# Optimization experiments

Measured on AMD Instinct MI355X. Metric: run time of the kernel, lower is better.

The kernel has to match this reference:

```python
import jax, jax.numpy as jnp
import numpy as np

DIM = 512
NUM_HEADS = 8
HEAD_DIM = DIM // NUM_HEADS
MAX_SIZE = 128


def setup_inputs() -> dict:
    key = jax.random.key(0)
    ks = jax.random.split(key, 13)
    B, C, H, W = 4, DIM, 128, 128
    inp = {
        "x": jax.random.normal(ks[0], (B, C, H, W), jnp.float32),
        "q_w": jax.random.normal(ks[1], (DIM, DIM), jnp.float32) * 0.02,
        "q_b": jax.random.normal(ks[2], (DIM,), jnp.float32) * 0.02,
        "k_w": jax.random.normal(ks[3], (DIM, DIM), jnp.float32) * 0.02,
        "k_b": jax.random.normal(ks[4], (DIM,), jnp.float32) * 0.02,
        "v_w": jax.random.normal(ks[5], (DIM, DIM), jnp.float32) * 0.02,
        "v_b": jax.random.normal(ks[6], (DIM,), jnp.float32) * 0.02,
        "o_w": jax.random.normal(ks[7], (DIM, DIM), jnp.float32) * 0.02,
        "o_b": jax.random.normal(ks[8], (DIM,), jnp.float32) * 0.02,
        "pos_q": jax.random.normal(ks[9], (1, NUM_HEADS, MAX_SIZE, HEAD_DIM), jnp.float32),
        "pos_k": jax.random.normal(ks[10], (1, NUM_HEADS, MAX_SIZE, HEAD_DIM), jnp.float32),
        "pos_v": jax.random.normal(ks[11], (1, NUM_HEADS, MAX_SIZE, HEAD_DIM), jnp.float32),
        "g_q": jnp.ones((1,), jnp.float32),
        "g_k": jnp.ones((1,), jnp.float32),
        "g_v1": jnp.ones((1,), jnp.float32),
        "g_v2": jnp.ones((1,), jnp.float32),
    }
    return inp


def _gated_axial_attn(x, q_w, q_b, k_w, k_b, v_w, v_b, o_w, o_b,
                      pos_q, pos_k, pos_v, g_q, g_k, g_v1, g_v2):
    B, C, H, W = x.shape
    nh, hd = NUM_HEADS, C // NUM_HEADS
    scale = hd ** (-0.5)
    # axis='width': attend along W for each (B,H) row
    xf = jnp.transpose(x, (0, 2, 3, 1)).reshape(B * H, W, C)  # (BH, W, C)

    def proj(w, b):
        y = xf @ w.T + b                       # (BH, W, C)
        return jnp.transpose(y.reshape(B * H, W, nh, hd), (0, 2, 1, 3))  # (BH, nh, W, hd)

    q = proj(q_w, q_b)
    k = proj(k_w, k_b)
    v = proj(v_w, v_b)

    pq = pos_q[0, :, :W, :]  # (nh, W, hd)
    pk = pos_k[0, :, :W, :]
    pv = pos_v[0, :, :W, :]

    # scores[i,j] = q_i.k_j + g_q * q_i.pq_j + g_k * pk_i.k_j, all scaled
    scores = jnp.einsum('bnid,bnjd->bnij', q, k)
    scores = scores + g_q[0] * jnp.einsum('bnid,njd->bnij', q, pq)
    scores = scores + g_k[0] * jnp.einsum('nid,bnjd->bnij', pk, k)
    attn = jax.nn.softmax(scores * scale, axis=-1)  # (BH, nh, W, W)

    vmix = g_v1[0] * v + g_v2[0] * pv[None]        # (BH, nh, W, hd)
    out = jnp.einsum('bnij,bnjd->bnid', attn, vmix)
    out = jnp.transpose(out, (0, 2, 1, 3)).reshape(B * H, W, C)
    out = out @ o_w.T + o_b
    return jnp.transpose(out.reshape(B, H, W, C), (0, 3, 1, 2))  # (B, C, H, W)


def reference(x, q_w, q_b, k_w, k_b, v_w, v_b, o_w, o_b,
              pos_q, pos_k, pos_v, g_q, g_k, g_v1, g_v2):
    return _gated_axial_attn(x, q_w, q_b, k_w, k_b, v_w, v_b, o_w, o_b,
                             pos_q, pos_k, pos_v, g_q, g_k, g_v1, g_v2)
```

## Files before the change

kernel.cpp:

```cpp
#include <hip/hip_runtime.h>

typedef __bf16 bf16;
typedef __attribute__((ext_vector_type(8))) __bf16 bf16x8;
typedef __attribute__((ext_vector_type(4))) __bf16 bf16x4;
typedef __attribute__((ext_vector_type(4))) float fvec4;

#define MFMA16(a, b, c) __builtin_amdgcn_mfma_f32_16x16x32_bf16(a, b, c, 0, 0, 0)

__device__ __forceinline__ void glds16(const bf16* g, bf16* l) {
  __builtin_amdgcn_global_load_lds(
      (const __attribute__((address_space(1))) void*)g,
      (__attribute__((address_space(3))) void*)l, 16, 0, 0);
}

__device__ inline fvec4 zero4() { fvec4 z = {0.f, 0.f, 0.f, 0.f}; return z; }

#define PREP_ELEMS 1245184

__global__ __launch_bounds__(512) void prep_kernel(
    const float* __restrict__ qw, const float* __restrict__ kw,
    const float* __restrict__ vw, const float* __restrict__ ow,
    const float* __restrict__ pq, const float* __restrict__ pk,
    const float* __restrict__ pv, bf16* __restrict__ dst)
{
  int i = (blockIdx.x * 512 + threadIdx.x) * 4;
  const float* s;
  if      (i < 262144)  s = qw + i;
  else if (i < 524288)  s = kw + (i - 262144);
  else if (i < 786432)  s = vw + (i - 524288);
  else if (i < 1048576) s = ow + (i - 786432);
  else if (i < 1114112) s = pq + (i - 1048576);
  else if (i < 1179648) s = pk + (i - 1114112);
  else                  s = pv + (i - 1179648);
  fvec4 v = *(const fvec4*)s;
  bf16x4 o = { (bf16)v[0], (bf16)v[1], (bf16)v[2], (bf16)v[3] };
  *(bf16x4*)(dst + i) = o;
}

__global__ __launch_bounds__(256) void xpose_kernel(
    const float* __restrict__ x, bf16* __restrict__ xt, int bh0)
{
  __shared__ float Xs[64 * 133];
  const int cb = blockIdx.x, lb = blockIdx.y;
  const int bh = bh0 + lb, b = bh >> 7, h = bh & 127;
  const int t = threadIdx.x;
  const float* xb = x + (size_t)b * 8388608 + (size_t)(cb * 64) * 16384 + h * 128;
  #pragma unroll
  for (int it = 0; it < 8; ++it) {
    int idx = it * 256 + t;
    int c = idx >> 5, w4 = (idx & 31) << 2;
    fvec4 v = *(const fvec4*)(xb + (size_t)c * 16384 + w4);
    #pragma unroll
    for (int j = 0; j < 4; ++j) Xs[c * 133 + w4 + j] = v[j];
  }
  __syncthreads();
  const int c0 = (t & 7) * 8, wsub = t >> 3;
  #pragma unroll
  for (int wb = 0; wb < 4; ++wb) {
    int w = wb * 32 + wsub;
    bf16x8 o;
    #pragma unroll
    for (int i = 0; i < 8; ++i) o[i] = (bf16)Xs[(c0 + i) * 133 + w];
    *(bf16x8*)(xt + ((size_t)lb * 128 + w) * 512 + cb * 64 + c0) = o;
  }
}

__global__ __launch_bounds__(256, 3) void qkvgemm_kernel(
    const bf16* __restrict__ xt, const bf16* __restrict__ wqkv,
    const float* __restrict__ q_b, const float* __restrict__ k_b,
    const float* __restrict__ v_b, bf16* __restrict__ qkvbuf)
{
  __shared__ bf16 As[128 * 64];
  __shared__ bf16 Bs[128 * 64];
  const int nwg = gridDim.x;
  int wg = blockIdx.x;
  if ((nwg & 7) == 0) wg = (wg & 7) * (nwg >> 3) + (wg >> 3);
  const int mt = wg / 12;
  const int nt0 = (wg - mt * 12) * 128;
  const int m0 = mt * 128;
  const int t = threadIdx.x;
  const int wv = t >> 6, lane = t & 63;
  const int lr = lane & 15, lg = lane >> 4;
  const int wm = wv >> 1, wn = wv & 1;
  const int srow = lane >> 3, c16 = lane & 7;

  fvec4 acc[4][4];
  #pragma unroll
  for (int i = 0; i < 4; ++i)
    #pragma unroll
    for (int j = 0; j < 4; ++j) acc[i][j] = zero4();

  for (int k0 = 0; k0 < 512; k0 += 64) {
    __syncthreads();
    #pragma unroll
    for (int j = 0; j < 4; ++j) {
      int seg = wv * 4 + j;
      int row = seg * 8 + srow;
      int cs = c16 ^ (row & 7);
      glds16(xt + (size_t)(m0 + row) * 512 + k0 + cs * 8, As + seg * 512);
      glds16(wqkv + (size_t)(nt0 + row) * 512 + k0 + cs * 8, Bs + seg * 512);
    }
    __syncthreads();
    #pragma unroll
    for (int kc = 0; kc < 2; ++kc) {
      bf16x8 af[4], bfv[4];
      #pragma unroll
      for (int mt2 = 0; mt2 < 4; ++mt2) {
        int row = wm * 64 + mt2 * 16 + lr;
        int cs = (kc * 4 + lg) ^ (row & 7);
        af[mt2] = *(const bf16x8*)(As + row * 64 + cs * 8);
      }
      #pragma unroll
      for (int nt = 0; nt < 4; ++nt) {
        int row = wn * 64 + nt * 16 + lr;
        int cs = (kc * 4 + lg) ^ (row & 7);
        bfv[nt] = *(const bf16x8*)(Bs + row * 64 + cs * 8);
      }
      #pragma unroll
      for (int mt2 = 0; mt2 < 4; ++mt2)
        #pragma unroll
        for (int nt = 0; nt < 4; ++nt)
          acc[mt2][nt] = MFMA16(af[mt2], bfv[nt], acc[mt2][nt]);
    }
  }
  #pragma unroll
  for (int nt = 0; nt < 4; ++nt) {
    int col = nt0 + wn * 64 + nt * 16 + lr;
    int cr = col & 511;
    const float* bias = (col < 512) ? q_b : ((col < 1024) ? k_b : v_b);
    float bv = bias[cr];
    #pragma unroll
    for (int mt2 = 0; mt2 < 4; ++mt2) {
      int mb = m0 + wm * 64 + mt2 * 16 + lg * 4;
      #pragma unroll
      for (int r = 0; r < 4; ++r)
        qkvbuf[(size_t)(mb + r) * 1536 + col] = (bf16)(acc[mt2][nt][r] + bv);
    }
  }
}

__global__ __launch_bounds__(512, 2) void attn_kernel(
    const bf16* __restrict__ qkvbuf, const bf16* __restrict__ posb,
    const float* __restrict__ g_q, const float* __restrict__ g_k,
    const float* __restrict__ g_v1, const float* __restrict__ g_v2,
    bf16* __restrict__ ao)
{
  __shared__ bf16 KP[128 * 136];
  __shared__ bf16 Vt[64 * 136];
  const int blk = blockIdx.x;
  const int lb = blk >> 3, n = blk & 7;
  const float gq = g_q[0], gk = g_k[0];
  const float gv1 = g_v1[0], gv2 = g_v2[0];
  const bf16* Qb = qkvbuf + (size_t)(lb * 128) * 1536 + n * 64;
  const bf16* Kb = Qb + 512;
  const bf16* Vb = Qb + 1024;
  const bf16* pqb = posb + (size_t)n * 8192;
  const bf16* pkb = posb + 65536 + (size_t)n * 8192;
  const bf16* pvb = posb + 131072 + (size_t)n * 8192;
  const int t = threadIdx.x;

  #pragma unroll
  for (int it = 0; it < 2; ++it) {
    int idx = it * 512 + t;
    int j = idx >> 3, d0 = (idx & 7) << 3;
    bf16x8 kv  = *(const bf16x8*)(Kb + (size_t)j * 1536 + d0);
    bf16x8 pq8 = *(const bf16x8*)(pqb + j * 64 + d0);
    bf16x8 r1;
    #pragma unroll
    for (int i = 0; i < 8; ++i) r1[i] = (bf16)((float)kv[i] + gq * (float)pq8[i]);
    *(bf16x8*)(&KP[j * 136 + d0]) = r1;
    *(bf16x8*)(&KP[j * 136 + 64 + d0]) = kv;
    bf16x8 vv  = *(const bf16x8*)(Vb + (size_t)j * 1536 + d0);
    bf16x8 pv8 = *(const bf16x8*)(pvb + j * 64 + d0);
    #pragma unroll
    for (int i = 0; i < 8; ++i)
      Vt[(d0 + i) * 136 + j] = (bf16)(gv1 * (float)vv[i] + gv2 * (float)pv8[i]);
  }
  __syncthreads();

  const int wv = t >> 6, l = t & 63, lr = l & 15, lg = l >> 4;
  const int i0 = wv * 16;

  fvec4 s[8];
  #pragma unroll
  for (int i = 0; i < 8; ++i) s[i] = zero4();
  for (int kc = 0; kc < 4; ++kc) {
    bf16x8 af;
    if (kc < 2) {
      af = *(const bf16x8*)(Qb + (size_t)(i0 + lr) * 1536 + kc * 32 + lg * 8);
    } else {
      bf16x8 raw = *(const bf16x8*)(pkb + (i0 + lr) * 64 + (kc - 2) * 32 + lg * 8);
      #pragma unroll
      for (int i = 0; i < 8; ++i) af[i] = (bf16)(gk * (float)raw[i]);
    }
    #pragma unroll
    for (int jt = 0; jt < 8; ++jt) {
      bf16x8 bfr = *(const bf16x8*)(&KP[(jt * 16 + lr) * 136 + kc * 32 + lg * 8]);
      s[jt] = MFMA16(af, bfr, s[jt]);
    }
  }

  const float scale = 0.125f;
  float inv[4];
  #pragma unroll
  for (int r = 0; r < 4; ++r) {
    float m = -1e30f;
    #pragma unroll
    for (int jt = 0; jt < 8; ++jt) m = fmaxf(m, s[jt][r]);
    #pragma unroll
    for (int off = 1; off < 16; off <<= 1) m = fmaxf(m, __shfl_xor(m, off));
    float sm = 0.f;
    #pragma unroll
    for (int jt = 0; jt < 8; ++jt) {
      float e = __expf((s[jt][r] - m) * scale);
      s[jt][r] = e;
      sm += e;
    }
    #pragma unroll
    for (int off = 1; off < 16; off <<= 1) sm += __shfl_xor(sm, off);
    inv[r] = 1.f / sm;
  }
  __syncthreads();
  #pragma unroll
  for (int r = 0; r < 4; ++r) {
    int i = i0 + lg * 4 + r;
    #pragma unroll
    for (int jt = 0; jt < 8; ++jt)
      KP[i * 136 + jt * 16 + lr] = (bf16)(s[jt][r] * inv[r]);
  }
  __syncthreads();

  fvec4 o[4];
  #pragma unroll
  for (int i = 0; i < 4; ++i) o[i] = zero4();
  for (int kc = 0; kc < 4; ++kc) {
    bf16x8 af = *(const bf16x8*)(&KP[(i0 + lr) * 136 + kc * 32 + lg * 8]);
    #pragma unroll
    for (int dt = 0; dt < 4; ++dt) {
      bf16x8 bfr = *(const bf16x8*)(&Vt[(dt * 16 + lr) * 136 + kc * 32 + lg * 8]);
      o[dt] = MFMA16(af, bfr, o[dt]);
    }
  }
  #pragma unroll
  for (int dt = 0; dt < 4; ++dt) {
    #pragma unroll
    for (int r = 0; r < 4; ++r) {
      int i = i0 + lg * 4 + r;
      ao[((size_t)lb * 128 + i) * 512 + n * 64 + dt * 16 + lr] = (bf16)o[dt][r];
    }
  }
}

__global__ __launch_bounds__(256, 3) void oproj_kernel(
    const bf16* __restrict__ ao, const bf16* __restrict__ wo,
    const float* __restrict__ o_b, float* __restrict__ out, int bh0)
{
  __shared__ bf16 As[128 * 64];
  __shared__ bf16 Bs[128 * 64];
  const int nwg = gridDim.x;
  int wg = blockIdx.x;
  if ((nwg & 7) == 0) wg = (wg & 7) * (nwg >> 3) + (wg >> 3);
  const int ct4 = wg & 3;
  const int lb = wg >> 2;
  const int bh = bh0 + lb, b = bh >> 7, h = bh & 127;
  const int t = threadIdx.x;
  const int wv = t >> 6, lane = t & 63;
  const int lr = lane & 15, lg = lane >> 4;
  const int wm = wv >> 1, wn = wv & 1;
  const int srow = lane >> 3, c16 = lane & 7;

  fvec4 acc[4][4];
  #pragma unroll
  for (int i = 0; i < 4; ++i)
    #pragma unroll
    for (int j = 0; j < 4; ++j) acc[i][j] = zero4();

  for (int k0 = 0; k0 < 512; k0 += 64) {
    __syncthreads();
    #pragma unroll
    for (int j = 0; j < 4; ++j) {
      int seg = wv * 4 + j;
      int row = seg * 8 + srow;
      int cs = c16 ^ (row & 7);
      glds16(wo + (size_t)(ct4 * 128 + row) * 512 + k0 + cs * 8, As + seg * 512);
      glds16(ao + ((size_t)lb * 128 + row) * 512 + k0 + cs * 8, Bs + seg * 512);
    }
    __syncthreads();
    #pragma unroll
    for (int kc = 0; kc < 2; ++kc) {
      bf16x8 af[4], bfv[4];
      #pragma unroll
      for (int mt = 0; mt < 4; ++mt) {
        int row = wm * 64 + mt * 16 + lr;
        int cs = (kc * 4 + lg) ^ (row & 7);
        af[mt] = *(const bf16x8*)(As + row * 64 + cs * 8);
      }
      #pragma unroll
      for (int nt = 0; nt < 4; ++nt) {
        int row = wn * 64 + nt * 16 + lr;
        int cs = (kc * 4 + lg) ^ (row & 7);
        bfv[nt] = *(const bf16x8*)(Bs + row * 64 + cs * 8);
      }
      #pragma unroll
      for (int mt = 0; mt < 4; ++mt)
        #pragma unroll
        for (int nt = 0; nt < 4; ++nt)
          acc[mt][nt] = MFMA16(af[mt], bfv[nt], acc[mt][nt]);
    }
  }
  #pragma unroll
  for (int mt = 0; mt < 4; ++mt) {
    #pragma unroll
    for (int r = 0; r < 4; ++r) {
      int co = ct4 * 128 + wm * 64 + mt * 16 + lg * 4 + r;
      float bv = o_b[co];
      size_t ob = ((size_t)(b * 512 + co) * 128 + h) * 128;
      #pragma unroll
      for (int nt = 0; nt < 4; ++nt) {
        int w = wn * 64 + nt * 16 + lr;
        out[ob + w] = acc[mt][nt][r] + bv;
      }
    }
  }
}

extern "C" void kernel_launch(void* const* d_in, const int* in_sizes, int n_in,
                              void* d_out, int out_size, void* d_ws, size_t ws_size,
                              hipStream_t stream) {
  const float* x    = (const float*)d_in[0];
  const float* q_w  = (const float*)d_in[1];
  const float* q_b  = (const float*)d_in[2];
  const float* k_w  = (const float*)d_in[3];
  const float* k_b  = (const float*)d_in[4];
  const float* v_w  = (const float*)d_in[5];
  const float* v_b  = (const float*)d_in[6];
  const float* o_w  = (const float*)d_in[7];
  const float* o_b  = (const float*)d_in[8];
  const float* pos_q = (const float*)d_in[9];
  const float* pos_k = (const float*)d_in[10];
  const float* pos_v = (const float*)d_in[11];
  const float* g_q  = (const float*)d_in[12];
  const float* g_k  = (const float*)d_in[13];
  const float* g_v1 = (const float*)d_in[14];
  const float* g_v2 = (const float*)d_in[15];
  float* out = (float*)d_out;

  bf16* prep = (bf16*)d_ws;
  bf16* wqkv = prep;
  bf16* wo   = prep + 786432;
  bf16* posb = prep + 1048576;

  bf16* rest = prep + PREP_ELEMS;
  size_t avail = (ws_size > (size_t)PREP_ELEMS * 2) ? ws_size - (size_t)PREP_ELEMS * 2 : 0;
  const size_t per_bh = (size_t)(65536 + 196608) * sizeof(bf16);
  int nbh = (int)(avail / per_bh);
  if (nbh > 128) nbh = 128;
  if (nbh < 1) nbh = 1;

  bf16* xt = rest;
  bf16* qkvbuf = xt + (size_t)nbh * 65536;

  prep_kernel<<<608, 512, 0, stream>>>(q_w, k_w, v_w, o_w, pos_q, pos_k, pos_v, prep);

  for (int bh0 = 0; bh0 < 512; bh0 += nbh) {
    int cur = (512 - bh0 < nbh) ? (512 - bh0) : nbh;
    xpose_kernel<<<dim3(8, cur), 256, 0, stream>>>(x, xt, bh0);
    qkvgemm_kernel<<<cur * 12, 256, 0, stream>>>(xt, wqkv, q_b, k_b, v_b, qkvbuf);
    attn_kernel<<<cur * 8, 512, 0, stream>>>(qkvbuf, posb, g_q, g_k, g_v1, g_v2, xt);
    oproj_kernel<<<cur * 4, 256, 0, stream>>>(xt, wo, o_b, out, bh0);
  }
}
```

Baseline: 510.5 us.

## Fuse QKV projection GEMM into per-head attention kernel, drop qkv buffer

Merges the QKV GEMM and attention into one kernel. Each block computes the Q, K and V projections for one (row, head) pair straight into registers, then stages them through shared memory for attention, so the bf16 qkv intermediate never goes to global memory. The freed workspace lets the chunk size grow to cover all 512 rows, which means fewer launches. The trade-off is that each block loads the x tile separately for every head (8x redundant A loads), and the kernel uses more registers and shared memory per block.

```diff
diff --git a/kernel.cpp b/kernel.cpp
--- a/kernel.cpp
+++ b/kernel.cpp
@@ -65,129 +65,114 @@
   }
 }
 
-__global__ __launch_bounds__(256, 3) void qkvgemm_kernel(
+__global__ __launch_bounds__(512, 4) void qkvattn_kernel(
     const bf16* __restrict__ xt, const bf16* __restrict__ wqkv,
     const float* __restrict__ q_b, const float* __restrict__ k_b,
-    const float* __restrict__ v_b, bf16* __restrict__ qkvbuf)
-{
-  __shared__ bf16 As[128 * 64];
-  __shared__ bf16 Bs[128 * 64];
-  const int nwg = gridDim.x;
-  int wg = blockIdx.x;
-  if ((nwg & 7) == 0) wg = (wg & 7) * (nwg >> 3) + (wg >> 3);
-  const int mt = wg / 12;
-  const int nt0 = (wg - mt * 12) * 128;
-  const int m0 = mt * 128;
-  const int t = threadIdx.x;
-  const int wv = t >> 6, lane = t & 63;
-  const int lr = lane & 15, lg = lane >> 4;
-  const int wm = wv >> 1, wn = wv & 1;
-  const int srow = lane >> 3, c16 = lane & 7;
-
-  fvec4 acc[4][4];
-  #pragma unroll
-  for (int i = 0; i < 4; ++i)
-    #pragma unroll
-    for (int j = 0; j < 4; ++j) acc[i][j] = zero4();
-
-  for (int k0 = 0; k0 < 512; k0 += 64) {
-    __syncthreads();
-    #pragma unroll
-    for (int j = 0; j < 4; ++j) {
-      int seg = wv * 4 + j;
-      int row = seg * 8 + srow;
-      int cs = c16 ^ (row & 7);
-      glds16(xt + (size_t)(m0 + row) * 512 + k0 + cs * 8, As + seg * 512);
-      glds16(wqkv + (size_t)(nt0 + row) * 512 + k0 + cs * 8, Bs + seg * 512);
-    }
-    __syncthreads();
-    #pragma unroll
-    for (int kc = 0; kc < 2; ++kc) {
-      bf16x8 af[4], bfv[4];
-      #pragma unroll
-      for (int mt2 = 0; mt2 < 4; ++mt2) {
-        int row = wm * 64 + mt2 * 16 + lr;
-        int cs = (kc * 4 + lg) ^ (row & 7);
-        af[mt2] = *(const bf16x8*)(As + row * 64 + cs * 8);
-      }
-      #pragma unroll
-      for (int nt = 0; nt < 4; ++nt) {
-        int row = wn * 64 + nt * 16 + lr;
-        int cs = (kc * 4 + lg) ^ (row & 7);
-        bfv[nt] = *(const bf16x8*)(Bs + row * 64 + cs * 8);
-      }
-      #pragma unroll
-      for (int mt2 = 0; mt2 < 4; ++mt2)
-        #pragma unroll
-        for (int nt = 0; nt < 4; ++nt)
-          acc[mt2][nt] = MFMA16(af[mt2], bfv[nt], acc[mt2][nt]);
-    }
-  }
-  #pragma unroll
-  for (int nt = 0; nt < 4; ++nt) {
-    int col = nt0 + wn * 64 + nt * 16 + lr;
-    int cr = col & 511;
-    const float* bias = (col < 512) ? q_b : ((col < 1024) ? k_b : v_b);
-    float bv = bias[cr];
-    #pragma unroll
-    for (int mt2 = 0; mt2 < 4; ++mt2) {
-      int mb = m0 + wm * 64 + mt2 * 16 + lg * 4;
-      #pragma unroll
-      for (int r = 0; r < 4; ++r)
-        qkvbuf[(size_t)(mb + r) * 1536 + col] = (bf16)(acc[mt2][nt][r] + bv);
-    }
-  }
-}
-
-__global__ __launch_bounds__(512, 2) void attn_kernel(
-    const bf16* __restrict__ qkvbuf, const bf16* __restrict__ posb,
+    const float* __restrict__ v_b, const bf16* __restrict__ posb,
     const float* __restrict__ g_q, const float* __restrict__ g_k,
     const float* __restrict__ g_v1, const float* __restrict__ g_v2,
     bf16* __restrict__ ao)
 {
-  __shared__ bf16 KP[128 * 136];
-  __shared__ bf16 Vt[64 * 136];
-  const int blk = blockIdx.x;
-  const int lb = blk >> 3, n = blk & 7;
-  const float gq = g_q[0], gk = g_k[0];
-  const float gv1 = g_v1[0], gv2 = g_v2[0];
-  const bf16* Qb = qkvbuf + (size_t)(lb * 128) * 1536 + n * 64;
-  const bf16* Kb = Qb + 512;
-  const bf16* Vb = Qb + 1024;
+  __shared__ bf16 SM[26624];
+  bf16* As = SM;
+  bf16* Bs = SM + 8192;
+  bf16* Qs = SM;
+  bf16* KP = SM + 9216;
+  bf16* Vt = SM;
+
+  const int nwg = gridDim.x;
+  int wg = blockIdx.x;
+  wg = (wg & 7) * (nwg >> 3) + (wg >> 3);
+  const int lb = wg >> 3, n = wg & 7;
+
+  const int t = threadIdx.x;
+  const int wv = t >> 6, lane = t & 63;
+  const int lr = lane & 15, lg = lane >> 4;
+  const int srow = lane >> 3, c16 = lane & 7;
+
+  fvec4 acc[12];
+  #pragma unroll
+  for (int i = 0; i < 12; ++i) acc[i] = zero4();
+
+  const bf16* asrc[2];
+  const bf16* bsrc[3];
+  #pragma unroll
+  for (int j = 0; j < 2; ++j) {
+    int seg = wv * 2 + j;
+    int row = seg * 8 + srow;
+    int cs = c16 ^ (row & 7);
+    asrc[j] = xt + (size_t)(lb * 128 + row) * 512 + cs * 8;
+  }
+  #pragma unroll
+  for (int j = 0; j < 3; ++j) {
+    int seg = wv * 3 + j;
+    int row = seg * 8 + srow;
+    int grow = ((row >> 6) << 9) + (n << 6) + (row & 63);
+    int cs = c16 ^ (row & 7);
+    bsrc[j] = wqkv + (size_t)grow * 512 + cs * 8;
+  }
+
+  for (int k0 = 0; k0 < 512; k0 += 64) {
+    __syncthreads();
+    #pragma unroll
+    for (int j = 0; j < 2; ++j)
+      glds16(asrc[j] + k0, As + (wv * 2 + j) * 512);
+    #pragma unroll
+    for (int j = 0; j < 3; ++j)
+      glds16(bsrc[j] + k0, Bs + (wv * 3 + j) * 512);
+    __syncthreads();
+    #pragma unroll
+    for (int kc = 0; kc < 2; ++kc) {
+      int arow = wv * 16 + lr;
+      int acs = (kc * 4 + lg) ^ (arow & 7);
+      bf16x8 af = *(const bf16x8*)(As + arow * 64 + acs * 8);
+      #pragma unroll
+      for (int nt = 0; nt < 12; ++nt) {
+        int brow = nt * 16 + lr;
+        int bcs = (kc * 4 + lg) ^ (brow & 7);
+        bf16x8 bfv = *(const bf16x8*)(Bs + brow * 64 + bcs * 8);
+        acc[nt] = MFMA16(af, bfv, acc[nt]);
+      }
+    }
+  }
+  __syncthreads();
+
+  const float gq = g_q[0], gk = g_k[0], gv1 = g_v1[0], gv2 = g_v2[0];
   const bf16* pqb = posb + (size_t)n * 8192;
   const bf16* pkb = posb + 65536 + (size_t)n * 8192;
   const bf16* pvb = posb + 131072 + (size_t)n * 8192;
-  const int t = threadIdx.x;
-
-  #pragma unroll
-  for (int it = 0; it < 2; ++it) {
-    int idx = it * 512 + t;
-    int j = idx >> 3, d0 = (idx & 7) << 3;
-    bf16x8 kv  = *(const bf16x8*)(Kb + (size_t)j * 1536 + d0);
-    bf16x8 pq8 = *(const bf16x8*)(pqb + j * 64 + d0);
-    bf16x8 r1;
-    #pragma unroll
-    for (int i = 0; i < 8; ++i) r1[i] = (bf16)((float)kv[i] + gq * (float)pq8[i]);
-    *(bf16x8*)(&KP[j * 136 + d0]) = r1;
-    *(bf16x8*)(&KP[j * 136 + 64 + d0]) = kv;
-    bf16x8 vv  = *(const bf16x8*)(Vb + (size_t)j * 1536 + d0);
-    bf16x8 pv8 = *(const bf16x8*)(pvb + j * 64 + d0);
-    #pragma unroll
-    for (int i = 0; i < 8; ++i)
-      Vt[(d0 + i) * 136 + j] = (bf16)(gv1 * (float)vv[i] + gv2 * (float)pv8[i]);
-  }
-  __syncthreads();
-
-  const int wv = t >> 6, l = t & 63, lr = l & 15, lg = l >> 4;
   const int i0 = wv * 16;
 
+  #pragma unroll
+  for (int nt = 0; nt < 4; ++nt) {
+    float bq = q_b[n * 64 + nt * 16 + lr];
+    #pragma unroll
+    for (int r = 0; r < 4; ++r)
+      Qs[(i0 + lg * 4 + r) * 72 + nt * 16 + lr] = (bf16)(acc[nt][r] + bq);
+  }
+  #pragma unroll
+  for (int nt = 0; nt < 4; ++nt) {
+    int d = nt * 16 + lr;
+    float bk = k_b[n * 64 + d];
+    #pragma unroll
+    for (int r = 0; r < 4; ++r) {
+      int jr = i0 + lg * 4 + r;
+      float kv = acc[4 + nt][r] + bk;
+      float pqv = (float)pqb[jr * 64 + d];
+      KP[jr * 136 + d]      = (bf16)(kv + gq * pqv);
+      KP[jr * 136 + 64 + d] = (bf16)kv;
+    }
+  }
+  __syncthreads();
+
   fvec4 s[8];
   #pragma unroll
   for (int i = 0; i < 8; ++i) s[i] = zero4();
+  #pragma unroll
   for (int kc = 0; kc < 4; ++kc) {
     bf16x8 af;
     if (kc < 2) {
-      af = *(const bf16x8*)(Qb + (size_t)(i0 + lr) * 1536 + kc * 32 + lg * 8);
+      af = *(const bf16x8*)(Qs + (i0 + lr) * 72 + kc * 32 + lg * 8);
     } else {
       bf16x8 raw = *(const bf16x8*)(pkb + (i0 + lr) * 64 + (kc - 2) * 32 + lg * 8);
       #pragma unroll
@@ -195,7 +180,7 @@
     }
     #pragma unroll
     for (int jt = 0; jt < 8; ++jt) {
-      bf16x8 bfr = *(const bf16x8*)(&KP[(jt * 16 + lr) * 136 + kc * 32 + lg * 8]);
+      bf16x8 bfr = *(const bf16x8*)(KP + (jt * 16 + lr) * 136 + kc * 32 + lg * 8);
       s[jt] = MFMA16(af, bfr, s[jt]);
     }
   }
@@ -221,6 +206,7 @@
     inv[r] = 1.f / sm;
   }
   __syncthreads();
+
   #pragma unroll
   for (int r = 0; r < 4; ++r) {
     int i = i0 + lg * 4 + r;
@@ -228,16 +214,28 @@
     for (int jt = 0; jt < 8; ++jt)
       KP[i * 136 + jt * 16 + lr] = (bf16)(s[jt][r] * inv[r]);
   }
+  #pragma unroll
+  for (int nt = 0; nt < 4; ++nt) {
+    int d = nt * 16 + lr;
+    float bv = v_b[n * 64 + d];
+    #pragma unroll
+    for (int r = 0; r < 4; ++r) {
+      int jr = i0 + lg * 4 + r;
+      Vt[d * 136 + jr] =
+          (bf16)(gv1 * (acc[8 + nt][r] + bv) + gv2 * (float)pvb[jr * 64 + d]);
+    }
+  }
   __syncthreads();
 
   fvec4 o[4];
   #pragma unroll
   for (int i = 0; i < 4; ++i) o[i] = zero4();
+  #pragma unroll
   for (int kc = 0; kc < 4; ++kc) {
-    bf16x8 af = *(const bf16x8*)(&KP[(i0 + lr) * 136 + kc * 32 + lg * 8]);
+    bf16x8 af = *(const bf16x8*)(KP + (i0 + lr) * 136 + kc * 32 + lg * 8);
     #pragma unroll
     for (int dt = 0; dt < 4; ++dt) {
-      bf16x8 bfr = *(const bf16x8*)(&Vt[(dt * 16 + lr) * 136 + kc * 32 + lg * 8]);
+      bf16x8 bfr = *(const bf16x8*)(Vt + (dt * 16 + lr) * 136 + kc * 32 + lg * 8);
       o[dt] = MFMA16(af, bfr, o[dt]);
     }
   }
@@ -352,21 +350,21 @@
 
   bf16* rest = prep + PREP_ELEMS;
   size_t avail = (ws_size > (size_t)PREP_ELEMS * 2) ? ws_size - (size_t)PREP_ELEMS * 2 : 0;
-  const size_t per_bh = (size_t)(65536 + 196608) * sizeof(bf16);
+  const size_t per_bh = (size_t)(65536 + 65536) * sizeof(bf16);
   int nbh = (int)(avail / per_bh);
-  if (nbh > 128) nbh = 128;
+  if (nbh > 512) nbh = 512;
   if (nbh < 1) nbh = 1;
 
   bf16* xt = rest;
-  bf16* qkvbuf = xt + (size_t)nbh * 65536;
+  bf16* ao = xt + (size_t)nbh * 65536;
 
   prep_kernel<<<608, 512, 0, stream>>>(q_w, k_w, v_w, o_w, pos_q, pos_k, pos_v, prep);
 
   for (int bh0 = 0; bh0 < 512; bh0 += nbh) {
     int cur = (512 - bh0 < nbh) ? (512 - bh0) : nbh;
     xpose_kernel<<<dim3(8, cur), 256, 0, stream>>>(x, xt, bh0);
-    qkvgemm_kernel<<<cur * 12, 256, 0, stream>>>(xt, wqkv, q_b, k_b, v_b, qkvbuf);
-    attn_kernel<<<cur * 8, 512, 0, stream>>>(qkvbuf, posb, g_q, g_k, g_v1, g_v2, xt);
-    oproj_kernel<<<cur * 4, 256, 0, stream>>>(xt, wo, o_b, out, bh0);
-  }
-}
+    qkvattn_kernel<<<cur * 8, 512, 0, stream>>>(xt, wqkv, q_b, k_b, v_b, posb,
+                                                g_q, g_k, g_v1, g_v2, ao);
+    oproj_kernel<<<cur * 4, 256, 0, stream>>>(ao, wo, o_b, out, bh0);
+  }
+}
```

Result: no change. 510.5 us (-0.0%).
